# Performance work log

Hardware: AMD Instinct MI355X
Metric: run time of the kernel (lower is better)

## Reference

```python
import jax, jax.numpy as jnp
import numpy as np

EMBED_DIM = 1024
NUM_HEADS = 16
HEAD_DIM = EMBED_DIM // NUM_HEADS


def setup_inputs() -> dict:
    key = jax.random.key(0)
    ks = jax.random.split(key, 9)
    B, S, D = 4, 2048, EMBED_DIM
    s = 1.0 / np.sqrt(D)
    return {
        "x": jax.random.normal(ks[0], (B, S, D), dtype=jnp.float32),
        "Wq": jax.random.uniform(ks[1], (D, D), jnp.float32, -s, s),
        "bq": jax.random.uniform(ks[2], (D,), jnp.float32, -s, s),
        "Wk": jax.random.uniform(ks[3], (D, D), jnp.float32, -s, s),
        "bk": jax.random.uniform(ks[4], (D,), jnp.float32, -s, s),
        "Wv": jax.random.uniform(ks[5], (D, D), jnp.float32, -s, s),
        "bv": jax.random.uniform(ks[6], (D,), jnp.float32, -s, s),
        "Wo": jax.random.uniform(ks[7], (D, D), jnp.float32, -s, s),
        "bo": jax.random.uniform(ks[8], (D,), jnp.float32, -s, s),
    }


def reference(x, Wq, bq, Wk, bk, Wv, bv, Wo, bo):
    B, S, D = x.shape
    H, Hd = NUM_HEADS, HEAD_DIM

    def proj(W, b):
        # torch Linear: x @ W.T + b; reshape to [B, H, S, Hd]
        y = jnp.einsum('bsd,ed->bse', x, W) + b
        return y.reshape(B, S, H, Hd).transpose(0, 2, 1, 3)

    Q = proj(Wq, bq)
    K = proj(Wk, bk)
    V = proj(Wv, bv)
    scores = jnp.einsum('bhqd,bhkd->bhqk', Q, K) / np.sqrt(Hd).astype(jnp.float32)
    attn = jax.nn.softmax(scores, axis=-1)
    out = jnp.einsum('bhqk,bhkd->bhqd', attn, V)
    out = out.transpose(0, 2, 1, 3).reshape(B, S, D)
    return jnp.einsum('bsd,ed->bse', out, Wo) + bo
```

## Files before the change

kernel.cpp:

```cpp
#include <hip/hip_runtime.h>
#include <stdint.h>

typedef unsigned short u16;
typedef _Float16 f16;
typedef __fp16 fp16x2 __attribute__((ext_vector_type(2)));
typedef f16 f16x4 __attribute__((ext_vector_type(4)));
typedef f16 f16x8 __attribute__((ext_vector_type(8)));
typedef float f32x4 __attribute__((ext_vector_type(4)));
typedef u16 u16x4v __attribute__((ext_vector_type(4)));
typedef uint32_t u32x2 __attribute__((ext_vector_type(2)));

#define MFMAH  __builtin_amdgcn_mfma_f32_16x16x32_f16
#define MFMA16 __builtin_amdgcn_mfma_f32_16x16x16f16

__device__ __forceinline__ void gload16(const void* g, void* l) {
    __builtin_amdgcn_global_load_lds(
        (const __attribute__((address_space(1))) uint32_t*)g,
        (__attribute__((address_space(3))) uint32_t*)l, 16, 0, 0);
}

__global__ __launch_bounds__(256) void convert_x(const float4* __restrict__ x,
                                                 f16x8* __restrict__ o) {
    int i = blockIdx.x * 256 + threadIdx.x;
    float4 a = x[2 * i], b = x[2 * i + 1];
    f16x8 h;
    h[0] = (f16)a.x; h[1] = (f16)a.y; h[2] = (f16)a.z; h[3] = (f16)a.w;
    h[4] = (f16)b.x; h[5] = (f16)b.y; h[6] = (f16)b.z; h[7] = (f16)b.w;
    o[i] = h;
}

__global__ __launch_bounds__(256) void convert_w(const float4* __restrict__ Wq,
                                                 const float4* __restrict__ Wk,
                                                 const float4* __restrict__ Wv,
                                                 const float4* __restrict__ Wo,
                                                 f16x8* __restrict__ hi,
                                                 f16x8* __restrict__ lo) {
    int gi = blockIdx.x * 256 + threadIdx.x;
    int wsel = gi >> 17;
    int li = gi & 131071;
    const float4* src = (wsel == 0) ? Wq : (wsel == 1) ? Wk : (wsel == 2) ? Wv : Wo;
    float4 a = src[2 * li], b = src[2 * li + 1];
    float v[8] = {a.x, a.y, a.z, a.w, b.x, b.y, b.z, b.w};
    f16x8 h;
#pragma unroll
    for (int j = 0; j < 8; ++j) h[j] = (f16)v[j];
    hi[gi] = h;
    if (wsel == 3) {
        f16x8 l;
#pragma unroll
        for (int j = 0; j < 8; ++j) l[j] = (f16)(v[j] - (float)h[j]);
        lo[gi] = l;
    }
}

__global__ __launch_bounds__(512, 4)
void gemm_qkv(const f16* __restrict__ A,
              const f16* __restrict__ Whi,
              const float* __restrict__ b0, const float* __restrict__ b1,
              const float* __restrict__ b2,
              f16* __restrict__ oq, f16* __restrict__ ok, f16* __restrict__ ov) {
    __shared__ f16 ldsA[256 * 64];
    __shared__ f16 ldsW[128 * 64];
    const int t = threadIdx.x;
    const int lane = t & 63, quad = lane >> 4, l16 = lane & 15;
    const int wid = t >> 6;
    const int wsel = blockIdx.x >> 3;
    const int bm = blockIdx.y * 256;
    const int bn = (blockIdx.x & 7) * 128;
    const int wm = (wid >> 1) * 64, wn = (wid & 1) * 64;
    const f16* Wh = Whi + (size_t)wsel * 1048576;
    const float* bias = (wsel == 0) ? b0 : (wsel == 1) ? b1 : b2;

    f32x4 acc[4][4] = {};

    for (int kt = 0; kt < 16; ++kt) {
        __syncthreads();
        const int k0 = kt * 64;
#pragma unroll
        for (int c = 0; c < 4; ++c) {
            const int u = c * 512 + t;
            const int r = u >> 3, cc = u & 7;
            const int sc = cc ^ (r & 7);
            gload16(A + (size_t)(bm + r) * 1024 + k0 + sc * 8, &ldsA[u * 8]);
        }
#pragma unroll
        for (int c = 0; c < 2; ++c) {
            const int u = c * 512 + t;
            const int r = u >> 3, cc = u & 7;
            const int sc = cc ^ (r & 7);
            gload16(Wh + (size_t)(bn + r) * 1024 + k0 + sc * 8, &ldsW[u * 8]);
        }
        __syncthreads();

#pragma unroll
        for (int kq = 0; kq < 2; ++kq) {
            f16x8 bh[4];
            const int chb = kq * 4 + quad;
            const int ch = chb ^ (l16 & 7);
#pragma unroll
            for (int i = 0; i < 4; ++i) {
                const int rb = wn + i * 16 + l16;
                bh[i] = *(const f16x8*)&ldsW[rb * 64 + ch * 8];
            }
#pragma unroll
            for (int mi = 0; mi < 4; ++mi) {
                const int ra = wm + mi * 16 + l16;
                const f16x8 af = *(const f16x8*)&ldsA[ra * 64 + ch * 8];
#pragma unroll
                for (int ni = 0; ni < 4; ++ni)
                    acc[mi][ni] = MFMAH(af, bh[ni], acc[mi][ni], 0, 0, 0);
            }
        }
    }

#pragma unroll
    for (int ni = 0; ni < 4; ++ni) {
        const int e = bn + wn + ni * 16 + l16;
        const float bv = bias[e];
        const int h = e >> 6, d = e & 63;
#pragma unroll
        for (int mi = 0; mi < 4; ++mi) {
            const int row0 = bm + wm + mi * 16 + quad * 4;
            if (wsel == 2) {
                const int b = row0 >> 11, s0 = row0 & 2047;
                ushort4 pk;
                f16 p0 = (f16)(acc[mi][ni][0] + bv);
                f16 p1 = (f16)(acc[mi][ni][1] + bv);
                f16 p2 = (f16)(acc[mi][ni][2] + bv);
                f16 p3 = (f16)(acc[mi][ni][3] + bv);
                pk.x = __builtin_bit_cast(u16, p0);
                pk.y = __builtin_bit_cast(u16, p1);
                pk.z = __builtin_bit_cast(u16, p2);
                pk.w = __builtin_bit_cast(u16, p3);
                *(ushort4*)(ov + ((size_t)((b * 16 + h) * 64 + d)) * 2048 + s0) = pk;
            } else {
                f16* dst = (wsel == 0) ? oq : ok;
#pragma unroll
                for (int r = 0; r < 4; ++r) {
                    const int row = row0 + r;
                    const int b = row >> 11, s = row & 2047;
                    float v = acc[mi][ni][r] + bv;
                    if (wsel == 0) v *= 0.18033688f;
                    dst[((size_t)((b * 16 + h) * 2048 + s)) * 64 + d] = (f16)v;
                }
            }
        }
    }
}

__global__ __launch_bounds__(256, 2)
void gemm_o(const f16* __restrict__ A,
            const f16* __restrict__ Wh, const f16* __restrict__ Wl,
            const float* __restrict__ bias, float* __restrict__ ofp) {
    __shared__ f16 ldsA[128 * 64];
    __shared__ f16 ldsW[2][128 * 64];
    const int t = threadIdx.x;
    const int lane = t & 63, quad = lane >> 4, l16 = lane & 15;
    const int wid = t >> 6;
    const int bm = blockIdx.y * 128, bn = blockIdx.x * 128;
    const int wm = (wid >> 1) * 64, wn = (wid & 1) * 64;

    f32x4 acc[4][4] = {};

    for (int kt = 0; kt < 16; ++kt) {
        __syncthreads();
        const int k0 = kt * 64;
#pragma unroll
        for (int c = 0; c < 4; ++c) {
            const int u = c * 256 + t;
            const int r = u >> 3, cc = u & 7;
            const int sc = cc ^ (r & 7);
            gload16(A + (size_t)(bm + r) * 1024 + k0 + sc * 8, &ldsA[u * 8]);
        }
#pragma unroll
        for (int p = 0; p < 2; ++p) {
            const f16* Ws = p ? Wl : Wh;
#pragma unroll
            for (int c = 0; c < 4; ++c) {
                const int u = c * 256 + t;
                const int r = u >> 3, cc = u & 7;
                const int sc = cc ^ (r & 7);
                gload16(Ws + (size_t)(bn + r) * 1024 + k0 + sc * 8, &ldsW[p][u * 8]);
            }
        }
        __syncthreads();

#pragma unroll
        for (int kq = 0; kq < 2; ++kq) {
            f16x8 bh[4], bl[4];
            const int ch = (kq * 4 + quad) ^ (l16 & 7);
#pragma unroll
            for (int i = 0; i < 4; ++i) {
                const int rb = wn + i * 16 + l16;
                bh[i] = *(const f16x8*)&ldsW[0][rb * 64 + ch * 8];
                bl[i] = *(const f16x8*)&ldsW[1][rb * 64 + ch * 8];
            }
#pragma unroll
            for (int mi = 0; mi < 4; ++mi) {
                const int ra = wm + mi * 16 + l16;
                const f16x8 af = *(const f16x8*)&ldsA[ra * 64 + ch * 8];
#pragma unroll
                for (int ni = 0; ni < 4; ++ni) {
                    acc[mi][ni] = MFMAH(af, bh[ni], acc[mi][ni], 0, 0, 0);
                    acc[mi][ni] = MFMAH(af, bl[ni], acc[mi][ni], 0, 0, 0);
                }
            }
        }
    }

#pragma unroll
    for (int ni = 0; ni < 4; ++ni) {
        const int e = bn + wn + ni * 16 + l16;
        const float bv = bias[e];
#pragma unroll
        for (int mi = 0; mi < 4; ++mi) {
            const int row0 = bm + wm + mi * 16 + quad * 4;
#pragma unroll
            for (int r = 0; r < 4; ++r)
                ofp[(size_t)(row0 + r) * 1024 + e] = acc[mi][ni][r] + bv;
        }
    }
}

__global__ __launch_bounds__(512, 4)
void attn_fused(const f16* __restrict__ Q, const f16* __restrict__ K,
                const f16* __restrict__ Vt, f16* __restrict__ AO) {
    __shared__ f16 Kt[2][128 * 64];
    __shared__ f16 Vs[2][64 * 128];
    const int t = threadIdx.x, wid = t >> 6, lane = t & 63;
    const int quad = lane >> 4, l16 = lane & 15;
    const int sw7 = l16 & 7;
    const int bh = blockIdx.x;
    const int q0 = blockIdx.y * 256;
    const size_t base = (size_t)bh * (2048 * 64);

    const u16x4v o4 = {0x3C00, 0x3C00, 0x3C00, 0x3C00};
    const f16x4 ONES4 = __builtin_bit_cast(f16x4, o4);

    f16x8 qf[2][2];
#pragma unroll
    for (int s = 0; s < 2; ++s) {
        const int qrow = q0 + wid * 32 + s * 16 + l16;
        qf[s][0] = *(const f16x8*)(Q + base + (size_t)qrow * 64 + quad * 8);
        qf[s][1] = *(const f16x8*)(Q + base + (size_t)qrow * 64 + 32 + quad * 8);
    }

    f32x4 of[2][4] = {};
    f32x4 rs[2] = {};

    auto STAGE = [&](int bf, int kt) {
#pragma unroll
        for (int c = 0; c < 2; ++c) {
            const int u = c * 512 + t;
            const int row = u >> 3, cc = u & 7;
            const int sc = cc ^ (row & 7);
            gload16(K + base + (size_t)(kt * 128 + row) * 64 + sc * 8, &Kt[bf][u * 8]);
        }
#pragma unroll
        for (int c = 0; c < 2; ++c) {
            const int u = c * 512 + t;
            const int row = u >> 4, cc = u & 15;
            const int sc = cc ^ (row & 15);
            gload16(Vt + base + (size_t)row * 2048 + kt * 128 + sc * 8, &Vs[bf][u * 8]);
        }
    };

    STAGE(0, 0);
    __syncthreads();

    for (int kt = 0; kt < 16; ++kt) {
        const int bf = kt & 1;
        if (kt < 15) STAGE(bf ^ 1, kt + 1);

#pragma unroll
        for (int kk = 0; kk < 4; ++kk) {
            f16x4 pfq[2][2];
#pragma unroll
            for (int nn = 0; nn < 2; ++nn) {
                const int krow = (kk * 2 + nn) * 16 + l16;
                const f16x8 kb0 = *(const f16x8*)&Kt[bf][krow * 64 + (quad ^ sw7) * 8];
                const f16x8 kb1 = *(const f16x8*)&Kt[bf][krow * 64 + ((4 | quad) ^ sw7) * 8];
#pragma unroll
                for (int s = 0; s < 2; ++s) {
                    f32x4 sf = {};
                    sf = MFMAH(kb0, qf[s][0], sf, 0, 0, 0);
                    sf = MFMAH(kb1, qf[s][1], sf, 0, 0, 0);
                    const float p0 = __builtin_amdgcn_exp2f(sf[0]);
                    const float p1 = __builtin_amdgcn_exp2f(sf[1]);
                    const float p2 = __builtin_amdgcn_exp2f(sf[2]);
                    const float p3 = __builtin_amdgcn_exp2f(sf[3]);
                    u32x2 pw;
                    pw[0] = __builtin_bit_cast(uint32_t, __builtin_amdgcn_cvt_pkrtz(p0, p1));
                    pw[1] = __builtin_bit_cast(uint32_t, __builtin_amdgcn_cvt_pkrtz(p2, p3));
                    pfq[nn][s] = __builtin_bit_cast(f16x4, pw);
                }
            }
#pragma unroll
            for (int di = 0; di < 4; ++di) {
                const int row = di * 16 + l16;
#pragma unroll
                for (int nn = 0; nn < 2; ++nn) {
                    const int col = kk * 32 + nn * 16 + quad * 4;
                    const int chunk = (col >> 3) ^ (row & 15);
                    const f16x4 vb4 = *(const f16x4*)&Vs[bf][row * 128 + chunk * 8 + (quad & 1) * 4];
#pragma unroll
                    for (int s = 0; s < 2; ++s)
                        of[s][di] = MFMA16(vb4, pfq[nn][s], of[s][di], 0, 0, 0);
                }
            }
#pragma unroll
            for (int nn = 0; nn < 2; ++nn)
#pragma unroll
                for (int s = 0; s < 2; ++s)
                    rs[s] = MFMA16(ONES4, pfq[nn][s], rs[s], 0, 0, 0);
        }
        __syncthreads();
    }

    const int b = bh >> 4, h = bh & 15;
#pragma unroll
    for (int s = 0; s < 2; ++s) {
        const int qrow = q0 + wid * 32 + s * 16 + l16;
        const float inv = 1.0f / rs[s][0];
#pragma unroll
        for (int di = 0; di < 4; ++di) {
            const int e0 = h * 64 + di * 16 + quad * 4;
            ushort4 pk;
            f16 o0 = (f16)(of[s][di][0] * inv);
            f16 o1 = (f16)(of[s][di][1] * inv);
            f16 o2 = (f16)(of[s][di][2] * inv);
            f16 o3 = (f16)(of[s][di][3] * inv);
            pk.x = __builtin_bit_cast(u16, o0);
            pk.y = __builtin_bit_cast(u16, o1);
            pk.z = __builtin_bit_cast(u16, o2);
            pk.w = __builtin_bit_cast(u16, o3);
            *(ushort4*)(AO + (size_t)(b * 2048 + qrow) * 1024 + e0) = pk;
        }
    }
}

extern "C" void kernel_launch(void* const* d_in, const int* in_sizes, int n_in,
                              void* d_out, int out_size, void* d_ws, size_t ws_size,
                              hipStream_t stream) {
    const float* x  = (const float*)d_in[0];
    const float* Wq = (const float*)d_in[1];
    const float* bq = (const float*)d_in[2];
    const float* Wk = (const float*)d_in[3];
    const float* bk = (const float*)d_in[4];
    const float* Wv = (const float*)d_in[5];
    const float* bv = (const float*)d_in[6];
    const float* Wo = (const float*)d_in[7];
    const float* bo = (const float*)d_in[8];
    float* out = (float*)d_out;

    char* ws = (char*)d_ws;
    f16* XF  = (f16*)(ws);
    f16* WH  = (f16*)(ws + (16u << 20));
    f16* WL  = (f16*)(ws + (24u << 20));
    f16* QF  = (f16*)(ws + (32u << 20));
    f16* KF  = (f16*)(ws + (48u << 20));
    f16* VTF = (f16*)(ws + (64u << 20));
    f16* AOF = (f16*)(ws + (80u << 20));

    convert_x<<<4096, 256, 0, stream>>>((const float4*)x, (f16x8*)XF);
    convert_w<<<2048, 256, 0, stream>>>((const float4*)Wq, (const float4*)Wk,
                                        (const float4*)Wv, (const float4*)Wo,
                                        (f16x8*)WH, (f16x8*)WL);

    gemm_qkv<<<dim3(24, 32), 512, 0, stream>>>(XF, WH, bq, bk, bv, QF, KF, VTF);

    attn_fused<<<dim3(64, 8), 512, 0, stream>>>(QF, KF, VTF, AOF);

    gemm_o<<<dim3(8, 64), 256, 0, stream>>>(AOF, WH + 3145728, WL + 3145728, bo, out);
}
```

Measured before the change: 284.6 us.

## Double-buffer QKV GEMM with smaller M tile; compute softmax row sums in VALU

The QKV projection GEMM drops its M tile from 256 to 128 rows and double-buffers the LDS tiles. The next K-slice is now prefetched while MFMAs run on the current one, with one barrier per iteration, and the grid doubles to fill more CUs. In the attention kernel, the MFMA that summed probabilities against a ones vector is replaced by scalar adds of the f16 probabilities plus a cross-lane shuffle reduction at the end. This frees matrix-core issue slots but adds VALU work and converts each probability back to float.

```diff
diff --git a/kernel.cpp b/kernel.cpp
--- a/kernel.cpp
+++ b/kernel.cpp
@@ -7,7 +7,6 @@
 typedef f16 f16x4 __attribute__((ext_vector_type(4)));
 typedef f16 f16x8 __attribute__((ext_vector_type(8)));
 typedef float f32x4 __attribute__((ext_vector_type(4)));
-typedef u16 u16x4v __attribute__((ext_vector_type(4)));
 typedef uint32_t u32x2 __attribute__((ext_vector_type(2)));
 
 #define MFMAH  __builtin_amdgcn_mfma_f32_16x16x32_f16
@@ -59,58 +58,64 @@
               const float* __restrict__ b0, const float* __restrict__ b1,
               const float* __restrict__ b2,
               f16* __restrict__ oq, f16* __restrict__ ok, f16* __restrict__ ov) {
-    __shared__ f16 ldsA[256 * 64];
-    __shared__ f16 ldsW[128 * 64];
+    __shared__ f16 ldsA[2][128 * 64];
+    __shared__ f16 ldsW[2][128 * 64];
     const int t = threadIdx.x;
     const int lane = t & 63, quad = lane >> 4, l16 = lane & 15;
     const int wid = t >> 6;
     const int wsel = blockIdx.x >> 3;
-    const int bm = blockIdx.y * 256;
+    const int bm = blockIdx.y * 128;
     const int bn = (blockIdx.x & 7) * 128;
-    const int wm = (wid >> 1) * 64, wn = (wid & 1) * 64;
+    const int wm = (wid >> 1) * 32, wn = (wid & 1) * 64;
     const f16* Wh = Whi + (size_t)wsel * 1048576;
     const float* bias = (wsel == 0) ? b0 : (wsel == 1) ? b1 : b2;
 
-    f32x4 acc[4][4] = {};
-
-    for (int kt = 0; kt < 16; ++kt) {
-        __syncthreads();
+    f32x4 acc[2][4] = {};
+
+    auto STAGE = [&](int bf, int kt) {
         const int k0 = kt * 64;
-#pragma unroll
-        for (int c = 0; c < 4; ++c) {
-            const int u = c * 512 + t;
-            const int r = u >> 3, cc = u & 7;
-            const int sc = cc ^ (r & 7);
-            gload16(A + (size_t)(bm + r) * 1024 + k0 + sc * 8, &ldsA[u * 8]);
-        }
 #pragma unroll
         for (int c = 0; c < 2; ++c) {
             const int u = c * 512 + t;
             const int r = u >> 3, cc = u & 7;
             const int sc = cc ^ (r & 7);
-            gload16(Wh + (size_t)(bn + r) * 1024 + k0 + sc * 8, &ldsW[u * 8]);
-        }
-        __syncthreads();
+            gload16(A + (size_t)(bm + r) * 1024 + k0 + sc * 8, &ldsA[bf][u * 8]);
+        }
+#pragma unroll
+        for (int c = 0; c < 2; ++c) {
+            const int u = c * 512 + t;
+            const int r = u >> 3, cc = u & 7;
+            const int sc = cc ^ (r & 7);
+            gload16(Wh + (size_t)(bn + r) * 1024 + k0 + sc * 8, &ldsW[bf][u * 8]);
+        }
+    };
+
+    STAGE(0, 0);
+    __syncthreads();
+
+    for (int kt = 0; kt < 16; ++kt) {
+        const int bf = kt & 1;
+        if (kt < 15) STAGE(bf ^ 1, kt + 1);
 
 #pragma unroll
         for (int kq = 0; kq < 2; ++kq) {
             f16x8 bh[4];
-            const int chb = kq * 4 + quad;
-            const int ch = chb ^ (l16 & 7);
+            const int ch = (kq * 4 + quad) ^ (l16 & 7);
 #pragma unroll
             for (int i = 0; i < 4; ++i) {
                 const int rb = wn + i * 16 + l16;
-                bh[i] = *(const f16x8*)&ldsW[rb * 64 + ch * 8];
-            }
-#pragma unroll
-            for (int mi = 0; mi < 4; ++mi) {
+                bh[i] = *(const f16x8*)&ldsW[bf][rb * 64 + ch * 8];
+            }
+#pragma unroll
+            for (int mi = 0; mi < 2; ++mi) {
                 const int ra = wm + mi * 16 + l16;
-                const f16x8 af = *(const f16x8*)&ldsA[ra * 64 + ch * 8];
+                const f16x8 af = *(const f16x8*)&ldsA[bf][ra * 64 + ch * 8];
 #pragma unroll
                 for (int ni = 0; ni < 4; ++ni)
                     acc[mi][ni] = MFMAH(af, bh[ni], acc[mi][ni], 0, 0, 0);
             }
         }
+        __syncthreads();
     }
 
 #pragma unroll
@@ -119,7 +124,7 @@
         const float bv = bias[e];
         const int h = e >> 6, d = e & 63;
 #pragma unroll
-        for (int mi = 0; mi < 4; ++mi) {
+        for (int mi = 0; mi < 2; ++mi) {
             const int row0 = bm + wm + mi * 16 + quad * 4;
             if (wsel == 2) {
                 const int b = row0 >> 11, s0 = row0 & 2047;
@@ -234,9 +239,6 @@
     const int q0 = blockIdx.y * 256;
     const size_t base = (size_t)bh * (2048 * 64);
 
-    const u16x4v o4 = {0x3C00, 0x3C00, 0x3C00, 0x3C00};
-    const f16x4 ONES4 = __builtin_bit_cast(f16x4, o4);
-
     f16x8 qf[2][2];
 #pragma unroll
     for (int s = 0; s < 2; ++s) {
@@ -246,7 +248,7 @@
     }
 
     f32x4 of[2][4] = {};
-    f32x4 rs[2] = {};
+    float rsum[2] = {0.0f, 0.0f};
 
     auto STAGE = [&](int bf, int kt) {
 #pragma unroll
@@ -293,6 +295,8 @@
                     pw[0] = __builtin_bit_cast(uint32_t, __builtin_amdgcn_cvt_pkrtz(p0, p1));
                     pw[1] = __builtin_bit_cast(uint32_t, __builtin_amdgcn_cvt_pkrtz(p2, p3));
                     pfq[nn][s] = __builtin_bit_cast(f16x4, pw);
+                    rsum[s] += (float)pfq[nn][s][0] + (float)pfq[nn][s][1] +
+                               (float)pfq[nn][s][2] + (float)pfq[nn][s][3];
                 }
             }
 #pragma unroll
@@ -308,11 +312,6 @@
                         of[s][di] = MFMA16(vb4, pfq[nn][s], of[s][di], 0, 0, 0);
                 }
             }
-#pragma unroll
-            for (int nn = 0; nn < 2; ++nn)
-#pragma unroll
-                for (int s = 0; s < 2; ++s)
-                    rs[s] = MFMA16(ONES4, pfq[nn][s], rs[s], 0, 0, 0);
         }
         __syncthreads();
     }
@@ -320,8 +319,11 @@
     const int b = bh >> 4, h = bh & 15;
 #pragma unroll
     for (int s = 0; s < 2; ++s) {
+        float tot = rsum[s];
+        tot += __shfl_xor(tot, 16, 64);
+        tot += __shfl_xor(tot, 32, 64);
+        const float inv = 1.0f / tot;
         const int qrow = q0 + wid * 32 + s * 16 + l16;
-        const float inv = 1.0f / rs[s][0];
 #pragma unroll
         for (int di = 0; di < 4; ++di) {
             const int e0 = h * 64 + di * 16 + quad * 4;
@@ -367,7 +369,7 @@
                                         (const float4*)Wv, (const float4*)Wo,
                                         (f16x8*)WH, (f16x8*)WL);
 
-    gemm_qkv<<<dim3(24, 32), 512, 0, stream>>>(XF, WH, bq, bk, bv, QF, KF, VTF);
+    gemm_qkv<<<dim3(24, 64), 512, 0, stream>>>(XF, WH, bq, bk, bv, QF, KF, VTF);
 
     attn_fused<<<dim3(64, 8), 512, 0, stream>>>(QF, KF, VTF, AOF);
 
```

Result: slower. 297.5 us (+4.5%).

## Use 16x16x32 MFMA for PV in attention and enlarge gemm_o tiles

Applied to the files above, without the earlier changes.

In the attention kernel, the two 16x16x16 MFMAs per key chunk for P·V and for the row sums are merged into one 16x16x32 MFMA by packing two probability fragments into one f16x8 operand and concatenating the two V fragments. This halves the MFMA instruction count in the inner loop. Separately, gemm_o moves to 512-thread blocks with 256-row tiles, so each W tile loaded into LDS is reused across twice as many rows. The larger tile raises LDS use per block and halves the grid size.

```diff
diff --git a/kernel.cpp b/kernel.cpp
--- a/kernel.cpp
+++ b/kernel.cpp
@@ -7,11 +7,10 @@
 typedef f16 f16x4 __attribute__((ext_vector_type(4)));
 typedef f16 f16x8 __attribute__((ext_vector_type(8)));
 typedef float f32x4 __attribute__((ext_vector_type(4)));
-typedef u16 u16x4v __attribute__((ext_vector_type(4)));
-typedef uint32_t u32x2 __attribute__((ext_vector_type(2)));
+typedef u16 u16x8v __attribute__((ext_vector_type(8)));
+typedef uint32_t u32x4 __attribute__((ext_vector_type(4)));
 
 #define MFMAH  __builtin_amdgcn_mfma_f32_16x16x32_f16
-#define MFMA16 __builtin_amdgcn_mfma_f32_16x16x16f16
 
 __device__ __forceinline__ void gload16(const void* g, void* l) {
     __builtin_amdgcn_global_load_lds(
@@ -95,8 +94,7 @@
 #pragma unroll
         for (int kq = 0; kq < 2; ++kq) {
             f16x8 bh[4];
-            const int chb = kq * 4 + quad;
-            const int ch = chb ^ (l16 & 7);
+            const int ch = (kq * 4 + quad) ^ (l16 & 7);
 #pragma unroll
             for (int i = 0; i < 4; ++i) {
                 const int rb = wn + i * 16 + l16;
@@ -148,16 +146,16 @@
     }
 }
 
-__global__ __launch_bounds__(256, 2)
+__global__ __launch_bounds__(512, 4)
 void gemm_o(const f16* __restrict__ A,
             const f16* __restrict__ Wh, const f16* __restrict__ Wl,
             const float* __restrict__ bias, float* __restrict__ ofp) {
-    __shared__ f16 ldsA[128 * 64];
+    __shared__ f16 ldsA[256 * 64];
     __shared__ f16 ldsW[2][128 * 64];
     const int t = threadIdx.x;
     const int lane = t & 63, quad = lane >> 4, l16 = lane & 15;
     const int wid = t >> 6;
-    const int bm = blockIdx.y * 128, bn = blockIdx.x * 128;
+    const int bm = blockIdx.y * 256, bn = blockIdx.x * 128;
     const int wm = (wid >> 1) * 64, wn = (wid & 1) * 64;
 
     f32x4 acc[4][4] = {};
@@ -167,7 +165,7 @@
         const int k0 = kt * 64;
 #pragma unroll
         for (int c = 0; c < 4; ++c) {
-            const int u = c * 256 + t;
+            const int u = c * 512 + t;
             const int r = u >> 3, cc = u & 7;
             const int sc = cc ^ (r & 7);
             gload16(A + (size_t)(bm + r) * 1024 + k0 + sc * 8, &ldsA[u * 8]);
@@ -176,8 +174,8 @@
         for (int p = 0; p < 2; ++p) {
             const f16* Ws = p ? Wl : Wh;
 #pragma unroll
-            for (int c = 0; c < 4; ++c) {
-                const int u = c * 256 + t;
+            for (int c = 0; c < 2; ++c) {
+                const int u = c * 512 + t;
                 const int r = u >> 3, cc = u & 7;
                 const int sc = cc ^ (r & 7);
                 gload16(Ws + (size_t)(bn + r) * 1024 + k0 + sc * 8, &ldsW[p][u * 8]);
@@ -234,8 +232,8 @@
     const int q0 = blockIdx.y * 256;
     const size_t base = (size_t)bh * (2048 * 64);
 
-    const u16x4v o4 = {0x3C00, 0x3C00, 0x3C00, 0x3C00};
-    const f16x4 ONES4 = __builtin_bit_cast(f16x4, o4);
+    const u16x8v ou = {0x3C00, 0x3C00, 0x3C00, 0x3C00, 0x3C00, 0x3C00, 0x3C00, 0x3C00};
+    const f16x8 ONES8 = __builtin_bit_cast(f16x8, ou);
 
     f16x8 qf[2][2];
 #pragma unroll
@@ -274,7 +272,7 @@
 
 #pragma unroll
         for (int kk = 0; kk < 4; ++kk) {
-            f16x4 pfq[2][2];
+            u32x4 pws[2];
 #pragma unroll
             for (int nn = 0; nn < 2; ++nn) {
                 const int krow = (kk * 2 + nn) * 16 + l16;
@@ -289,30 +287,32 @@
                     const float p1 = __builtin_amdgcn_exp2f(sf[1]);
                     const float p2 = __builtin_amdgcn_exp2f(sf[2]);
                     const float p3 = __builtin_amdgcn_exp2f(sf[3]);
-                    u32x2 pw;
-                    pw[0] = __builtin_bit_cast(uint32_t, __builtin_amdgcn_cvt_pkrtz(p0, p1));
-                    pw[1] = __builtin_bit_cast(uint32_t, __builtin_amdgcn_cvt_pkrtz(p2, p3));
-                    pfq[nn][s] = __builtin_bit_cast(f16x4, pw);
+                    pws[s][nn * 2 + 0] = __builtin_bit_cast(uint32_t, __builtin_amdgcn_cvt_pkrtz(p0, p1));
+                    pws[s][nn * 2 + 1] = __builtin_bit_cast(uint32_t, __builtin_amdgcn_cvt_pkrtz(p2, p3));
                 }
             }
+            f16x8 pf8[2];
+#pragma unroll
+            for (int s = 0; s < 2; ++s)
+                pf8[s] = __builtin_bit_cast(f16x8, pws[s]);
+
 #pragma unroll
             for (int di = 0; di < 4; ++di) {
                 const int row = di * 16 + l16;
-#pragma unroll
-                for (int nn = 0; nn < 2; ++nn) {
-                    const int col = kk * 32 + nn * 16 + quad * 4;
-                    const int chunk = (col >> 3) ^ (row & 15);
-                    const f16x4 vb4 = *(const f16x4*)&Vs[bf][row * 128 + chunk * 8 + (quad & 1) * 4];
-#pragma unroll
-                    for (int s = 0; s < 2; ++s)
-                        of[s][di] = MFMA16(vb4, pfq[nn][s], of[s][di], 0, 0, 0);
-                }
-            }
-#pragma unroll
-            for (int nn = 0; nn < 2; ++nn)
+                const int col0 = kk * 32 + quad * 4;
+                const int ch0 = (col0 >> 3) ^ (row & 15);
+                const f16x4 v0 = *(const f16x4*)&Vs[bf][row * 128 + ch0 * 8 + (quad & 1) * 4];
+                const int col1 = col0 + 16;
+                const int ch1 = (col1 >> 3) ^ (row & 15);
+                const f16x4 v1 = *(const f16x4*)&Vs[bf][row * 128 + ch1 * 8 + (quad & 1) * 4];
+                const f16x8 vb8 = __builtin_shufflevector(v0, v1, 0, 1, 2, 3, 4, 5, 6, 7);
 #pragma unroll
                 for (int s = 0; s < 2; ++s)
-                    rs[s] = MFMA16(ONES4, pfq[nn][s], rs[s], 0, 0, 0);
+                    of[s][di] = MFMAH(vb8, pf8[s], of[s][di], 0, 0, 0);
+            }
+#pragma unroll
+            for (int s = 0; s < 2; ++s)
+                rs[s] = MFMAH(ONES8, pf8[s], rs[s], 0, 0, 0);
         }
         __syncthreads();
     }
@@ -371,5 +371,5 @@
 
     attn_fused<<<dim3(64, 8), 512, 0, stream>>>(QF, KF, VTF, AOF);
 
-    gemm_o<<<dim3(8, 64), 256, 0, stream>>>(AOF, WH + 3145728, WL + 3145728, bo, out);
-}
+    gemm_o<<<dim3(8, 32), 512, 0, stream>>>(AOF, WH + 3145728, WL + 3145728, bo, out);
+}
```

Result: slower. 295.9 us (+4.0%).
